# Performance work log

Measured on AMD Instinct MI355X. Metric: run time of the kernel, lower is better.

Reference implementation:

```python
import jax, jax.numpy as jnp
import numpy as np

B, D_DATA, D_DICT0, N_SAE, D_DICT = 2048, 768, 128, 128, 32


def _kaiming_uniform(key, shape, fan_in):
    # torch.nn.init.kaiming_uniform_ default: bound = sqrt(6 / fan_in) / sqrt(5-gain stuff) ~ use gain=sqrt(2)? match torch default a=sqrt(5) not needed; plain kaiming_uniform_ uses gain=sqrt(2): bound = sqrt(6/fan_in)*? Keep simple: bound = sqrt(6.0/fan_in)
    bound = np.sqrt(6.0 / fan_in)
    return jax.random.uniform(key, shape, jnp.float32, -bound, bound)


def setup_inputs() -> dict:
    key = jax.random.key(0)
    ks = jax.random.split(key, 6)
    x = jax.random.normal(ks[0], (B, D_DATA), jnp.float32)
    # top-level SAE params
    W_enc0 = _kaiming_uniform(ks[1], (D_DATA, D_DICT0), D_DATA)
    b_enc0 = jnp.zeros((D_DICT0,), jnp.float32)
    W_dec0 = _kaiming_uniform(ks[2], (D_DICT0, D_DATA), D_DICT0)
    W_dec0 = W_dec0 / jnp.linalg.norm(W_dec0, axis=-1, keepdims=True)
    b_dec0 = jnp.zeros((D_DATA,), jnp.float32)
    # sublayer (hierarchical) per-expert params
    W_enc1 = _kaiming_uniform(ks[3], (N_SAE, D_DATA, D_DICT), D_DATA)
    b_enc1 = jnp.zeros((N_SAE, D_DICT), jnp.float32)
    W_dec1 = _kaiming_uniform(ks[4], (N_SAE, D_DICT, D_DATA), D_DICT)
    W_dec1 = W_dec1 / jnp.linalg.norm(W_dec1, axis=-1, keepdims=True)
    b_dec1 = jnp.zeros((N_SAE, D_DATA), jnp.float32)
    return {"x": x, "W_enc0": W_enc0, "b_enc0": b_enc0, "W_dec0": W_dec0,
            "b_dec0": b_dec0, "W_enc1": W_enc1, "b_enc1": b_enc1,
            "W_dec1": W_dec1, "b_dec1": b_dec1}


def reference(x, W_enc0, b_enc0, W_dec0, b_dec0, W_enc1, b_enc1, W_dec1, b_dec1):
    # ---- sae_0 (standard SAE; scale/unscale are identity) ----
    acts0 = jax.nn.relu((x - b_dec0) @ W_enc0 + b_enc0)        # [B, D_DICT0]
    x0 = acts0 @ W_dec0 + b_dec0                               # [B, D_DATA]
    # ---- binary gate over experts (n_sae == d_dict0) ----
    gate = (acts0 > 0).astype(x.dtype)                         # [B, N_SAE]
    # ---- sublayer: gather-encode-decode-scatter, expressed densely with a
    # binary mask (gate only selects membership; gate value is not multiplied).
    # Avoid materializing [B, N_SAE, D_DATA] by distributing (x - b_dec1[j]):
    pre = (jnp.einsum('bd,jdk->bjk', x, W_enc1)
           - jnp.einsum('jd,jdk->jk', b_dec1, W_enc1)[None]
           + b_enc1[None])                                     # [B, N_SAE, D_DICT]
    acts1 = jax.nn.relu(pre) * gate[:, :, None]                # zero out ungated
    # scatter_add over experts: sum_j gated (acts1[b,j] @ W_dec1[j] + b_dec1[j])
    dec = jnp.einsum('bjk,jkd->bd', acts1, W_dec1) + gate @ b_dec1  # [B, D_DATA]
    return x0 + dec
```

## Files before the change

kernel.cpp:

```cpp
#include <hip/hip_runtime.h>
#include <hip/hip_bf16.h>
#include <stdint.h>

#define B_SZ   2048
#define DDATA  768
#define NSAE   128
#define NJK    4096
#define KA2    4352
#define SPLITK 2
#define KC2    2176
#define GZCH   8
#define GZW    96

typedef unsigned short u16;
typedef short bf16x8 __attribute__((ext_vector_type(8)));
typedef float f32x4  __attribute__((ext_vector_type(4)));

static __device__ __forceinline__ u16 f2bf(float f) {
  __hip_bfloat16 h = __float2bfloat16(f);
  return *reinterpret_cast<u16*>(&h);
}

static __device__ __forceinline__ void gload16(const u16* g, u16* l) {
  __builtin_amdgcn_global_load_lds(
      (const __attribute__((address_space(1))) unsigned int*)g,
      (__attribute__((address_space(3))) unsigned int*)l,
      16, 0, 0);
}

__global__ __launch_bounds__(256) void k_front(const float* __restrict__ x,
                                               const float* __restrict__ We0,
                                               const float* __restrict__ bd0,
                                               const float* __restrict__ We1,
                                               const float* __restrict__ bd1,
                                               const float* __restrict__ be1,
                                               const float* __restrict__ Wd1,
                                               const float* __restrict__ Wd0,
                                               u16* __restrict__ W1T,
                                               float* __restrict__ cv,
                                               u16* __restrict__ B2T,
                                               u16* __restrict__ xb,
                                               float* __restrict__ pp,
                                               float* __restrict__ xnp,
                                               float* __restrict__ wn) {
  __shared__ float smem[64 * 65];
  const int bid = blockIdx.x, t = threadIdx.x;
  if (bid < 128) {
    const int j = bid;
    float* ts  = smem;
    float* bds = smem + 64 * 33;
    float* red = smem + 64 * 33 + 64;
    const int k = t & 31, g = t >> 5;
    float cacc = 0.f;
    for (int db = 0; db < 12; ++db) {
      const float* src = We1 + (size_t)j * 24576 + db * 2048;
#pragma unroll
      for (int i = 0; i < 8; ++i) {
        int e = t + i * 256;
        ts[(e >> 5) * 33 + (e & 31)] = src[e];
      }
      if (t < 64) bds[t] = bd1[(size_t)j * DDATA + db * 64 + t];
      __syncthreads();
#pragma unroll
      for (int i = 0; i < 8; ++i) {
        int e = t + i * 256;
        int kk = e >> 6, d = e & 63;
        W1T[(size_t)(j * 32 + kk) * DDATA + db * 64 + d] = f2bf(ts[d * 33 + kk]);
      }
#pragma unroll
      for (int q = 0; q < 8; ++q) {
        int d = g + 8 * q;
        cacc += ts[d * 33 + k] * bds[d];
      }
      __syncthreads();
    }
    red[g * 32 + k] = cacc;
    __syncthreads();
    if (g == 0) {
      float s = 0.f;
#pragma unroll
      for (int q = 0; q < 8; ++q) s += red[q * 32 + k];
      cv[j * 32 + k] = be1[j * 32 + k] - s;
    }
  } else if (bid < 944) {
    const int e2 = bid - 128;
    const int rb = e2 / 12, dbk = e2 % 12;
    const float* src; int r0, base;
    if (rb < 64)      { src = Wd1; r0 = rb * 64;        base = 0;    }
    else if (rb < 66) { src = Wd0; r0 = (rb - 64) * 64; base = 4096; }
    else              { src = bd1; r0 = (rb - 66) * 64; base = 4224; }
    const int d0 = dbk * 64;
#pragma unroll
    for (int i = 0; i < 16; ++i) {
      int e = t + i * 256;
      int ri = e >> 6, di = e & 63;
      smem[ri * 65 + di] = src[(size_t)(r0 + ri) * DDATA + d0 + di];
    }
    __syncthreads();
#pragma unroll
    for (int i = 0; i < 16; ++i) {
      int e = t + i * 256;
      int di = e >> 6, ri = e & 63;
      B2T[(size_t)(d0 + di) * KA2 + base + r0 + ri] = f2bf(smem[ri * 65 + di]);
    }
  } else if (bid < 952) {
    const int wb = bid - 944;
    const int jj = wb * 16 + (t >> 4), s = t & 15;
    float acc = 0.f;
    for (int d = s; d < DDATA; d += 16) {
      float w = We0[(size_t)d * 128 + jj];
      acc += w * w;
    }
#pragma unroll
    for (int sh = 8; sh; sh >>= 1) acc += __shfl_xor(acc, sh, 64);
    if (s == 0) wn[jj] = sqrtf(acc);
  } else {
    const int bid2 = bid - 952;
    const int b0 = (bid2 & 63) * 32, z = bid2 >> 6;
    const int dbase = z * GZW;
    float* xs = smem;
#pragma unroll
    for (int i = 0; i < 3; ++i) {
      int idx = t + i * 256;
      int r = idx / 24, c4 = idx % 24;
      size_t go = (size_t)(b0 + r) * DDATA + dbase + c4 * 4;
      float4 v = *(const float4*)&x[go];
      ushort4 o;
      o.x = f2bf(v.x); o.y = f2bf(v.y); o.z = f2bf(v.z); o.w = f2bf(v.w);
      *(ushort4*)&xb[go] = o;
      float4 b4 = *(const float4*)&bd0[dbase + c4 * 4];
      v.x -= b4.x; v.y -= b4.y; v.z -= b4.z; v.w -= b4.w;
      *(float4*)&xs[r * GZW + c4 * 4] = v;
    }
    __syncthreads();
    const int jp = t & 63, rg = t >> 6;
    const int j0 = jp * 2;
    float ap[8][2], xq[8];
#pragma unroll
    for (int r = 0; r < 8; ++r) { ap[r][0] = ap[r][1] = xq[r] = 0.f; }
    for (int d = 0; d < GZW; d += 4) {
      float4 xv[8];
#pragma unroll
      for (int r = 0; r < 8; ++r)
        xv[r] = *(const float4*)&xs[(rg * 8 + r) * GZW + d];
#pragma unroll
      for (int dd = 0; dd < 4; ++dd) {
        float2 w2 = *(const float2*)&We0[(size_t)(dbase + d + dd) * 128 + j0];
#pragma unroll
        for (int r = 0; r < 8; ++r) {
          float xr = ((const float*)&xv[r])[dd];
          ap[r][0] += xr * w2.x;
          ap[r][1] += xr * w2.y;
          xq[r]    += xr * xr;
        }
      }
    }
#pragma unroll
    for (int r = 0; r < 8; ++r) {
      size_t o = ((size_t)z * B_SZ + b0 + rg * 8 + r) * 128 + j0;
      *(float2*)&pp[o] = make_float2(ap[r][0], ap[r][1]);
    }
    if (jp == 0) {
#pragma unroll
      for (int r = 0; r < 8; ++r)
        xnp[(size_t)z * B_SZ + b0 + rg * 8 + r] = xq[r];
    }
  }
}

__global__ __launch_bounds__(256) void k_gate2(const float* __restrict__ pp,
                                               const float* __restrict__ xnp,
                                               const float* __restrict__ wn,
                                               const float* __restrict__ be0,
                                               const float* __restrict__ x,
                                               const float* __restrict__ We0,
                                               const float* __restrict__ bd0,
                                               u16* __restrict__ A2) {
  const int i = blockIdx.x * 256 + threadIdx.x;
  const int b = i >> 7, j = i & 127;
  const int lane = threadIdx.x & 63;
  float p = be0[j], xn2 = 0.f;
#pragma unroll
  for (int z = 0; z < GZCH; ++z) {
    p   += pp[((size_t)z * B_SZ + b) * 128 + j];
    xn2 += xnp[(size_t)z * B_SZ + b];
  }
  const float tau = 1e-4f * sqrtf(xn2) * wn[j];
  size_t row = (size_t)b * KA2;
  A2[row + NJK + j]       = f2bf(p > 0.f ? p : 0.f);
  A2[row + NJK + 128 + j] = (p > 0.f) ? (u16)0x3F80 : (u16)0;
  unsigned long long mask = __ballot(fabsf(p) <= tau);
  while (mask) {
    int src = (int)__builtin_ctzll(mask);
    mask &= mask - 1;
    int bb = __shfl(b, src, 64), jj = __shfl(j, src, 64);
    double acc = 0.0;
#pragma unroll
    for (int tt = 0; tt < 12; ++tt) {
      int d = lane + tt * 64;
      acc += (double)(x[(size_t)bb * DDATA + d] - bd0[d]) *
             (double)We0[(size_t)d * 128 + jj];
    }
#pragma unroll
    for (int s = 32; s; s >>= 1) acc += __shfl_xor(acc, s, 64);
    if (lane == src) {
      double pd = acc + (double)be0[jj];
      size_t rw = (size_t)bb * KA2;
      A2[rw + NJK + jj]       = f2bf(pd > 0.0 ? (float)pd : 0.f);
      A2[rw + NJK + 128 + jj] = (pd > 0.0) ? (u16)0x3F80 : (u16)0;
    }
  }
}

template<int BM, int BN, int EPI>
__global__ __launch_bounds__(256) void k_gemm(const u16* __restrict__ A,
                                              const u16* __restrict__ Bm,
                                              int K, int Kc,
                                              float* __restrict__ outF,
                                              u16* __restrict__ A2,
                                              const float* __restrict__ cvec) {
  constexpr int WM = BM / 32, WN = BN / 32;
  __shared__ __align__(16) u16 As[BM * 64];
  __shared__ __align__(16) u16 Bs[BN * 64];
  __shared__ u16 gate_s[BM * 4];
  __shared__ float cv_s[BN];
  const int tid = threadIdx.x;
  const int bx = blockIdx.x, by = blockIdx.y, bz = blockIdx.z;
  const int kbase = bz * Kc;
  const u16* Ab = A  + (size_t)(by * BM) * K;
  const u16* Bb = Bm + (size_t)(bx * BN) * K;
  const int wave = tid >> 6, lane = tid & 63;
  const int wr = wave >> 1, wc = wave & 1;
  const int m0 = wr * (BM / 2), n0 = wc * (BN / 2);
  const int lm = lane & 15, qd = lane >> 4;

  if (EPI == 1) {
    for (int e = tid; e < BM * 4; e += 256) {
      int r = e >> 2, q = e & 3;
      gate_s[e] = A2[(size_t)(by * BM + r) * KA2 + NJK + 128 + bx * 4 + q];
    }
    for (int e = tid; e < BN; e += 256) cv_s[e] = cvec[bx * BN + e];
  }

  f32x4 acc[WM][WN];
  const f32x4 zero = {0.f, 0.f, 0.f, 0.f};
  for (int mi = 0; mi < WM; ++mi)
    for (int ni = 0; ni < WN; ++ni) acc[mi][ni] = zero;

  for (int k0 = kbase; k0 < kbase + Kc; k0 += 64) {
#pragma unroll
    for (int i = 0; i < BM / 32; ++i) {
      int id = tid + 256 * i;
      int row = id >> 3, u = id & 7;
      gload16(Ab + (size_t)row * K + k0 + ((u ^ (row & 7)) * 8), &As[id * 8]);
    }
#pragma unroll
    for (int i = 0; i < BN / 32; ++i) {
      int id = tid + 256 * i;
      int row = id >> 3, u = id & 7;
      gload16(Bb + (size_t)row * K + k0 + ((u ^ (row & 7)) * 8), &Bs[id * 8]);
    }
    __syncthreads();
#pragma unroll
    for (int s = 0; s < 2; ++s) {
      const int swz = ((s << 2) + qd) ^ (lm & 7);
      bf16x8 af[WM], bfv[WN];
#pragma unroll
      for (int mi = 0; mi < WM; ++mi)
        af[mi] = *(const bf16x8*)&As[(m0 + mi * 16 + lm) * 64 + swz * 8];
#pragma unroll
      for (int ni = 0; ni < WN; ++ni)
        bfv[ni] = *(const bf16x8*)&Bs[(n0 + ni * 16 + lm) * 64 + swz * 8];
#pragma unroll
      for (int mi = 0; mi < WM; ++mi)
#pragma unroll
        for (int ni = 0; ni < WN; ++ni)
          acc[mi][ni] = __builtin_amdgcn_mfma_f32_16x16x32_bf16(af[mi], bfv[ni],
                                                                acc[mi][ni], 0, 0, 0);
    }
    __syncthreads();
  }

  const int rb = qd * 4;
#pragma unroll
  for (int mi = 0; mi < WM; ++mi) {
#pragma unroll
    for (int ni = 0; ni < WN; ++ni) {
#pragma unroll
      for (int r = 0; r < 4; ++r) {
        int ml = m0 + mi * 16 + rb + r;
        int nl = n0 + ni * 16 + lm;
        int gm = by * BM + ml;
        int gn = bx * BN + nl;
        float v = acc[mi][ni][r];
        if (EPI == 1) {
          v += cv_s[nl];
          v = v > 0.f ? v : 0.f;
          u16 gbit = gate_s[ml * 4 + (nl >> 5)];
          v = gbit ? v : 0.f;
          float vn = __shfl_xor(v, 1, 64);
          if ((lm & 1) == 0) {
            unsigned pk = (unsigned)f2bf(v) | ((unsigned)f2bf(vn) << 16);
            *(unsigned*)&A2[(size_t)gm * KA2 + gn] = pk;
          }
        } else {
          outF[((size_t)bz * B_SZ + gm) * DDATA + gn] = v;
        }
      }
    }
  }
}

__global__ __launch_bounds__(256) void k_reduce(const float* __restrict__ part,
                                                const float* __restrict__ bias,
                                                float* __restrict__ out) {
  const int N4 = B_SZ * DDATA / 4;
  int i = blockIdx.x * 256 + threadIdx.x;
  const float4* p4 = (const float4*)part;
  float4 s = p4[i];
#pragma unroll
  for (int z = 1; z < SPLITK; ++z) {
    float4 t = p4[i + z * N4];
    s.x += t.x; s.y += t.y; s.z += t.z; s.w += t.w;
  }
  float4 b = ((const float4*)bias)[i % (DDATA / 4)];
  s.x += b.x; s.y += b.y; s.z += b.z; s.w += b.w;
  ((float4*)out)[i] = s;
}

extern "C" void kernel_launch(void* const* d_in, const int* in_sizes, int n_in,
                              void* d_out, int out_size, void* d_ws, size_t ws_size,
                              hipStream_t stream) {
  const float* x   = (const float*)d_in[0];
  const float* We0 = (const float*)d_in[1];
  const float* be0 = (const float*)d_in[2];
  const float* Wd0 = (const float*)d_in[3];
  const float* bd0 = (const float*)d_in[4];
  const float* We1 = (const float*)d_in[5];
  const float* be1 = (const float*)d_in[6];
  const float* Wd1 = (const float*)d_in[7];
  const float* bd1 = (const float*)d_in[8];
  float* out = (float*)d_out;

  uint8_t* ws = (uint8_t*)d_ws;
  size_t off = 0;
  auto carve = [&](size_t bytes) {
    uint8_t* p = ws + off;
    off += (bytes + 255) & ~(size_t)255;
    return p;
  };
  u16*    A2   = (u16*)carve((size_t)B_SZ * KA2 * 2);
  u16*    xb   = (u16*)carve((size_t)B_SZ * DDATA * 2);
  u16*    W1T  = (u16*)carve((size_t)NJK * DDATA * 2);
  u16*    B2T  = (u16*)carve((size_t)DDATA * KA2 * 2);
  float*  cv   = (float*)carve((size_t)NJK * 4);
  float*  part = (float*)carve((size_t)SPLITK * B_SZ * DDATA * 4);
  float*  pp   = (float*)carve((size_t)GZCH * B_SZ * 128 * 4);
  float*  xnp  = (float*)carve((size_t)GZCH * B_SZ * 4);
  float*  wn   = (float*)carve(128 * 4);

  k_front <<<1464, 256, 0, stream>>>(x, We0, bd0, We1, bd1, be1, Wd1, Wd0,
                                     W1T, cv, B2T, xb, pp, xnp, wn);
  k_gate2 <<<1024, 256, 0, stream>>>(pp, xnp, wn, be0, x, We0, bd0, A2);
  k_gemm<128, 128, 1><<<dim3(32, 16, 1), 256, 0, stream>>>(xb, W1T, DDATA, DDATA,
                                                           nullptr, A2, cv);
  k_gemm<32, 128, 2><<<dim3(6, 64, SPLITK), 256, 0, stream>>>(A2, B2T, KA2, KC2,
                                                              part, nullptr, nullptr);
  k_reduce<<<1536, 256, 0, stream>>>(part, bd0, out);
}
```

Before: 174.4 us.

## Fuse gate computation into front kernel, split W_enc1 transpose, remap GEMM blocks

Merges the separate partial-product and gate kernels into k_front: each block now computes full-row sae_0 pre-activations, norms and the fp64 near-zero recheck, writing acts and gate straight into A2. That removes one launch and the pp/xnp round trip. The W_enc1 transpose is split into three segments, with partial bias vectors summed in the GEMM epilogue. Both GEMMs get a 1D grid with a swizzled block-to-tile mapping for cache locality, and the second GEMM changes to 64-row tiles with split-K 4. In exchange the gate blocks run a long serial 768-length loop per thread, which may lengthen the front kernel.

```diff
diff --git a/kernel.cpp b/kernel.cpp
--- a/kernel.cpp
+++ b/kernel.cpp
@@ -7,10 +7,8 @@
 #define NSAE   128
 #define NJK    4096
 #define KA2    4352
-#define SPLITK 2
-#define KC2    2176
-#define GZCH   8
-#define GZW    96
+#define SPLITK 4
+#define KC2    1088
 
 typedef unsigned short u16;
 typedef short bf16x8 __attribute__((ext_vector_type(8)));
@@ -30,6 +28,7 @@
 
 __global__ __launch_bounds__(256) void k_front(const float* __restrict__ x,
                                                const float* __restrict__ We0,
+                                               const float* __restrict__ be0,
                                                const float* __restrict__ bd0,
                                                const float* __restrict__ We1,
                                                const float* __restrict__ bd1,
@@ -37,34 +36,127 @@
                                                const float* __restrict__ Wd1,
                                                const float* __restrict__ Wd0,
                                                u16* __restrict__ W1T,
-                                               float* __restrict__ cv,
+                                               float* __restrict__ cvp,
                                                u16* __restrict__ B2T,
                                                u16* __restrict__ xb,
-                                               float* __restrict__ pp,
-                                               float* __restrict__ xnp,
-                                               float* __restrict__ wn) {
-  __shared__ float smem[64 * 65];
+                                               u16* __restrict__ A2) {
+  __shared__ float smem[6280];
   const int bid = blockIdx.x, t = threadIdx.x;
-  if (bid < 128) {
-    const int j = bid;
+  if (bid < 256) {
+    const int b0 = bid * 8;
+    float* xs  = smem;
+    float* xns = smem + 6144;
+    float* wns = smem + 6152;
+#pragma unroll
+    for (int i = 0; i < 6; ++i) {
+      int idx = t + i * 256;
+      int r = idx / 192, c4 = idx % 192;
+      size_t go = (size_t)(b0 + r) * DDATA + c4 * 4;
+      float4 v = *(const float4*)&x[go];
+      ushort4 o;
+      o.x = f2bf(v.x); o.y = f2bf(v.y); o.z = f2bf(v.z); o.w = f2bf(v.w);
+      *(ushort4*)&xb[go] = o;
+      float4 b4 = *(const float4*)&bd0[c4 * 4];
+      v.x -= b4.x; v.y -= b4.y; v.z -= b4.z; v.w -= b4.w;
+      *(float4*)&xs[r * DDATA + c4 * 4] = v;
+    }
+    __syncthreads();
+    const int ln = t & 63, rg = t >> 6;
+#pragma unroll
+    for (int rr = 0; rr < 2; ++rr) {
+      int r = rg * 2 + rr;
+      float a = 0.f;
+#pragma unroll
+      for (int q = 0; q < 12; ++q) { float xv = xs[r * DDATA + ln + q * 64]; a += xv * xv; }
+#pragma unroll
+      for (int sh = 32; sh; sh >>= 1) a += __shfl_xor(a, sh, 64);
+      if (ln == 0) xns[r] = a;
+    }
+    const int j0 = ln * 2;
+    const float* xr0 = xs + (rg * 2) * DDATA;
+    const float* xr1 = xr0 + DDATA;
+    float pa0 = be0[j0], pa1 = be0[j0 + 1];
+    float pb0 = pa0, pb1 = pa1;
+    float wq0 = 0.f, wq1 = 0.f;
+#define GBODY(WQ)                                                         \
+    for (int d = 0; d < DDATA; d += 4) {                                  \
+      _Pragma("unroll")                                                   \
+      for (int dd = 0; dd < 4; ++dd) {                                    \
+        float2 w2 = *(const float2*)&We0[(size_t)(d + dd) * 128 + j0];    \
+        float a0 = xr0[d + dd], a1 = xr1[d + dd];                         \
+        pa0 += a0 * w2.x; pa1 += a0 * w2.y;                               \
+        pb0 += a1 * w2.x; pb1 += a1 * w2.y;                               \
+        if (WQ) { wq0 += w2.x * w2.x; wq1 += w2.y * w2.y; }               \
+      }                                                                   \
+    }
+    if (rg == 0) { GBODY(1); wns[j0] = sqrtf(wq0); wns[j0 + 1] = sqrtf(wq1); }
+    else         { GBODY(0); }
+#undef GBODY
+    __syncthreads();
+    const float sA = sqrtf(xns[rg * 2]), sB = sqrtf(xns[rg * 2 + 1]);
+    const float w0 = wns[j0], w1 = wns[j0 + 1];
+    const size_t rowA = (size_t)(b0 + rg * 2) * KA2;
+    const size_t rowB = rowA + KA2;
+    unsigned pka = (unsigned)f2bf(pa0 > 0.f ? pa0 : 0.f) |
+                   ((unsigned)f2bf(pa1 > 0.f ? pa1 : 0.f) << 16);
+    unsigned gka = (pa0 > 0.f ? 0x3F80u : 0u) | (pa1 > 0.f ? 0x3F800000u : 0u);
+    unsigned pkb = (unsigned)f2bf(pb0 > 0.f ? pb0 : 0.f) |
+                   ((unsigned)f2bf(pb1 > 0.f ? pb1 : 0.f) << 16);
+    unsigned gkb = (pb0 > 0.f ? 0x3F80u : 0u) | (pb1 > 0.f ? 0x3F800000u : 0u);
+    *(unsigned*)&A2[rowA + NJK + j0]       = pka;
+    *(unsigned*)&A2[rowA + NJK + 128 + j0] = gka;
+    *(unsigned*)&A2[rowB + NJK + j0]       = pkb;
+    *(unsigned*)&A2[rowB + NJK + 128 + j0] = gkb;
+    const float tA0 = 1e-4f * sA * w0, tA1 = 1e-4f * sA * w1;
+    const float tB0 = 1e-4f * sB * w0, tB1 = 1e-4f * sB * w1;
+#pragma unroll
+    for (int c = 0; c < 4; ++c) {
+      float pv = c == 0 ? pa0 : c == 1 ? pa1 : c == 2 ? pb0 : pb1;
+      float tv = c == 0 ? tA0 : c == 1 ? tA1 : c == 2 ? tB0 : tB1;
+      unsigned long long mask = __ballot(fabsf(pv) <= tv);
+      const int bb = b0 + rg * 2 + (c >> 1);
+      while (mask) {
+        int src = (int)__builtin_ctzll(mask);
+        mask &= mask - 1;
+        int jj = src * 2 + (c & 1);
+        double acc = 0.0;
+#pragma unroll
+        for (int q = 0; q < 12; ++q) {
+          int d = ln + q * 64;
+          acc += (double)(x[(size_t)bb * DDATA + d] - bd0[d]) *
+                 (double)We0[(size_t)d * 128 + jj];
+        }
+#pragma unroll
+        for (int sh = 32; sh; sh >>= 1) acc += __shfl_xor(acc, sh, 64);
+        if (ln == src) {
+          double pd = acc + (double)be0[jj];
+          size_t rw = (size_t)bb * KA2;
+          A2[rw + NJK + jj]       = f2bf(pd > 0.0 ? (float)pd : 0.f);
+          A2[rw + NJK + 128 + jj] = (pd > 0.0) ? (u16)0x3F80 : (u16)0;
+        }
+      }
+    }
+  } else if (bid < 640) {
+    const int e = bid - 256;
+    const int j = e & 127, seg = e >> 7;
     float* ts  = smem;
     float* bds = smem + 64 * 33;
     float* red = smem + 64 * 33 + 64;
     const int k = t & 31, g = t >> 5;
     float cacc = 0.f;
-    for (int db = 0; db < 12; ++db) {
+    for (int db = seg * 4; db < seg * 4 + 4; ++db) {
       const float* src = We1 + (size_t)j * 24576 + db * 2048;
 #pragma unroll
       for (int i = 0; i < 8; ++i) {
-        int e = t + i * 256;
-        ts[(e >> 5) * 33 + (e & 31)] = src[e];
+        int ee = t + i * 256;
+        ts[(ee >> 5) * 33 + (ee & 31)] = src[ee];
       }
       if (t < 64) bds[t] = bd1[(size_t)j * DDATA + db * 64 + t];
       __syncthreads();
 #pragma unroll
       for (int i = 0; i < 8; ++i) {
-        int e = t + i * 256;
-        int kk = e >> 6, d = e & 63;
+        int ee = t + i * 256;
+        int kk = ee >> 6, d = ee & 63;
         W1T[(size_t)(j * 32 + kk) * DDATA + db * 64 + d] = f2bf(ts[d * 33 + kk]);
       }
 #pragma unroll
@@ -80,10 +172,10 @@
       float s = 0.f;
 #pragma unroll
       for (int q = 0; q < 8; ++q) s += red[q * 32 + k];
-      cv[j * 32 + k] = be1[j * 32 + k] - s;
-    }
-  } else if (bid < 944) {
-    const int e2 = bid - 128;
+      cvp[seg * 4096 + j * 32 + k] = (seg == 0 ? be1[j * 32 + k] : 0.f) - s;
+    }
+  } else {
+    const int e2 = bid - 640;
     const int rb = e2 / 12, dbk = e2 % 12;
     const float* src; int r0, base;
     if (rb < 64)      { src = Wd1; r0 = rb * 64;        base = 0;    }
@@ -92,122 +184,16 @@
     const int d0 = dbk * 64;
 #pragma unroll
     for (int i = 0; i < 16; ++i) {
-      int e = t + i * 256;
-      int ri = e >> 6, di = e & 63;
+      int ee = t + i * 256;
+      int ri = ee >> 6, di = ee & 63;
       smem[ri * 65 + di] = src[(size_t)(r0 + ri) * DDATA + d0 + di];
     }
     __syncthreads();
 #pragma unroll
     for (int i = 0; i < 16; ++i) {
-      int e = t + i * 256;
-      int di = e >> 6, ri = e & 63;
+      int ee = t + i * 256;
+      int di = ee >> 6, ri = ee & 63;
       B2T[(size_t)(d0 + di) * KA2 + base + r0 + ri] = f2bf(smem[ri * 65 + di]);
-    }
-  } else if (bid < 952) {
-    const int wb = bid - 944;
-    const int jj = wb * 16 + (t >> 4), s = t & 15;
-    float acc = 0.f;
-    for (int d = s; d < DDATA; d += 16) {
-      float w = We0[(size_t)d * 128 + jj];
-      acc += w * w;
-    }
-#pragma unroll
-    for (int sh = 8; sh; sh >>= 1) acc += __shfl_xor(acc, sh, 64);
-    if (s == 0) wn[jj] = sqrtf(acc);
-  } else {
-    const int bid2 = bid - 952;
-    const int b0 = (bid2 & 63) * 32, z = bid2 >> 6;
-    const int dbase = z * GZW;
-    float* xs = smem;
-#pragma unroll
-    for (int i = 0; i < 3; ++i) {
-      int idx = t + i * 256;
-      int r = idx / 24, c4 = idx % 24;
-      size_t go = (size_t)(b0 + r) * DDATA + dbase + c4 * 4;
-      float4 v = *(const float4*)&x[go];
-      ushort4 o;
-      o.x = f2bf(v.x); o.y = f2bf(v.y); o.z = f2bf(v.z); o.w = f2bf(v.w);
-      *(ushort4*)&xb[go] = o;
-      float4 b4 = *(const float4*)&bd0[dbase + c4 * 4];
-      v.x -= b4.x; v.y -= b4.y; v.z -= b4.z; v.w -= b4.w;
-      *(float4*)&xs[r * GZW + c4 * 4] = v;
-    }
-    __syncthreads();
-    const int jp = t & 63, rg = t >> 6;
-    const int j0 = jp * 2;
-    float ap[8][2], xq[8];
-#pragma unroll
-    for (int r = 0; r < 8; ++r) { ap[r][0] = ap[r][1] = xq[r] = 0.f; }
-    for (int d = 0; d < GZW; d += 4) {
-      float4 xv[8];
-#pragma unroll
-      for (int r = 0; r < 8; ++r)
-        xv[r] = *(const float4*)&xs[(rg * 8 + r) * GZW + d];
-#pragma unroll
-      for (int dd = 0; dd < 4; ++dd) {
-        float2 w2 = *(const float2*)&We0[(size_t)(dbase + d + dd) * 128 + j0];
-#pragma unroll
-        for (int r = 0; r < 8; ++r) {
-          float xr = ((const float*)&xv[r])[dd];
-          ap[r][0] += xr * w2.x;
-          ap[r][1] += xr * w2.y;
-          xq[r]    += xr * xr;
-        }
-      }
-    }
-#pragma unroll
-    for (int r = 0; r < 8; ++r) {
-      size_t o = ((size_t)z * B_SZ + b0 + rg * 8 + r) * 128 + j0;
-      *(float2*)&pp[o] = make_float2(ap[r][0], ap[r][1]);
-    }
-    if (jp == 0) {
-#pragma unroll
-      for (int r = 0; r < 8; ++r)
-        xnp[(size_t)z * B_SZ + b0 + rg * 8 + r] = xq[r];
-    }
-  }
-}
-
-__global__ __launch_bounds__(256) void k_gate2(const float* __restrict__ pp,
-                                               const float* __restrict__ xnp,
-                                               const float* __restrict__ wn,
-                                               const float* __restrict__ be0,
-                                               const float* __restrict__ x,
-                                               const float* __restrict__ We0,
-                                               const float* __restrict__ bd0,
-                                               u16* __restrict__ A2) {
-  const int i = blockIdx.x * 256 + threadIdx.x;
-  const int b = i >> 7, j = i & 127;
-  const int lane = threadIdx.x & 63;
-  float p = be0[j], xn2 = 0.f;
-#pragma unroll
-  for (int z = 0; z < GZCH; ++z) {
-    p   += pp[((size_t)z * B_SZ + b) * 128 + j];
-    xn2 += xnp[(size_t)z * B_SZ + b];
-  }
-  const float tau = 1e-4f * sqrtf(xn2) * wn[j];
-  size_t row = (size_t)b * KA2;
-  A2[row + NJK + j]       = f2bf(p > 0.f ? p : 0.f);
-  A2[row + NJK + 128 + j] = (p > 0.f) ? (u16)0x3F80 : (u16)0;
-  unsigned long long mask = __ballot(fabsf(p) <= tau);
-  while (mask) {
-    int src = (int)__builtin_ctzll(mask);
-    mask &= mask - 1;
-    int bb = __shfl(b, src, 64), jj = __shfl(j, src, 64);
-    double acc = 0.0;
-#pragma unroll
-    for (int tt = 0; tt < 12; ++tt) {
-      int d = lane + tt * 64;
-      acc += (double)(x[(size_t)bb * DDATA + d] - bd0[d]) *
-             (double)We0[(size_t)d * 128 + jj];
-    }
-#pragma unroll
-    for (int s = 32; s; s >>= 1) acc += __shfl_xor(acc, s, 64);
-    if (lane == src) {
-      double pd = acc + (double)be0[jj];
-      size_t rw = (size_t)bb * KA2;
-      A2[rw + NJK + jj]       = f2bf(pd > 0.0 ? (float)pd : 0.f);
-      A2[rw + NJK + 128 + jj] = (pd > 0.0) ? (u16)0x3F80 : (u16)0;
     }
   }
 }
@@ -225,7 +211,18 @@
   __shared__ u16 gate_s[BM * 4];
   __shared__ float cv_s[BN];
   const int tid = threadIdx.x;
-  const int bx = blockIdx.x, by = blockIdx.y, bz = blockIdx.z;
+  int bx, by, bz;
+  {
+    const int h = blockIdx.x;
+    if (EPI == 1) {
+      const int l = (h & 7) * 64 + (h >> 3);
+      const int g2 = l >> 6, w = l & 63;
+      by = w >> 2; bx = (g2 << 2) + (w & 3); bz = 0;
+    } else {
+      const int l = (h & 7) * 96 + (h >> 3);
+      bx = l >> 7; const int r2 = l & 127; bz = r2 >> 5; by = r2 & 31;
+    }
+  }
   const int kbase = bz * Kc;
   const u16* Ab = A  + (size_t)(by * BM) * K;
   const u16* Bb = Bm + (size_t)(bx * BN) * K;
@@ -239,7 +236,8 @@
       int r = e >> 2, q = e & 3;
       gate_s[e] = A2[(size_t)(by * BM + r) * KA2 + NJK + 128 + bx * 4 + q];
     }
-    for (int e = tid; e < BN; e += 256) cv_s[e] = cvec[bx * BN + e];
+    for (int e = tid; e < BN; e += 256)
+      cv_s[e] = cvec[bx * BN + e] + cvec[4096 + bx * BN + e] + cvec[8192 + bx * BN + e];
   }
 
   f32x4 acc[WM][WN];
@@ -353,18 +351,14 @@
   u16*    xb   = (u16*)carve((size_t)B_SZ * DDATA * 2);
   u16*    W1T  = (u16*)carve((size_t)NJK * DDATA * 2);
   u16*    B2T  = (u16*)carve((size_t)DDATA * KA2 * 2);
-  float*  cv   = (float*)carve((size_t)NJK * 4);
+  float*  cvp  = (float*)carve((size_t)3 * NJK * 4);
   float*  part = (float*)carve((size_t)SPLITK * B_SZ * DDATA * 4);
-  float*  pp   = (float*)carve((size_t)GZCH * B_SZ * 128 * 4);
-  float*  xnp  = (float*)carve((size_t)GZCH * B_SZ * 4);
-  float*  wn   = (float*)carve(128 * 4);
-
-  k_front <<<1464, 256, 0, stream>>>(x, We0, bd0, We1, bd1, be1, Wd1, Wd0,
-                                     W1T, cv, B2T, xb, pp, xnp, wn);
-  k_gate2 <<<1024, 256, 0, stream>>>(pp, xnp, wn, be0, x, We0, bd0, A2);
-  k_gemm<128, 128, 1><<<dim3(32, 16, 1), 256, 0, stream>>>(xb, W1T, DDATA, DDATA,
-                                                           nullptr, A2, cv);
-  k_gemm<32, 128, 2><<<dim3(6, 64, SPLITK), 256, 0, stream>>>(A2, B2T, KA2, KC2,
-                                                              part, nullptr, nullptr);
+
+  k_front <<<1456, 256, 0, stream>>>(x, We0, be0, bd0, We1, bd1, be1, Wd1, Wd0,
+                                     W1T, cvp, B2T, xb, A2);
+  k_gemm<128, 128, 1><<<512, 256, 0, stream>>>(xb, W1T, DDATA, DDATA,
+                                               nullptr, A2, cvp);
+  k_gemm<64, 128, 2><<<768, 256, 0, stream>>>(A2, B2T, KA2, KC2,
+                                              part, nullptr, nullptr);
   k_reduce<<<1536, 256, 0, stream>>>(part, bd0, out);
 }
```

Result: slower. 184.2 us (+5.6%).
